# Kernel optimization log

Hardware: AMD Instinct MI355X
Metric: run time of the kernel (lower is better)

The kernel has to match this reference:

```python
import jax, jax.numpy as jnp
import numpy as np

L, D, H, HD, FF, V, R = 2, 2048, 16, 128, 5632, 32000, 16
B, S = 4, 512
LORA_SCALE = 1.4  # lora_alpha / r = (r*1.4)/r
TEMP = 0.05


def _rmsnorm(x, w):
    return x * jax.lax.rsqrt(jnp.mean(x * x, axis=-1, keepdims=True) + 1e-6) * w


def _rope(x):
    # x: [B, S, H, HD]
    half = HD // 2
    freqs = 1.0 / (10000.0 ** (jnp.arange(half, dtype=jnp.float32) / half))
    ang = jnp.arange(x.shape[1], dtype=jnp.float32)[:, None] * freqs[None, :]  # [S, half]
    cos = jnp.cos(ang)[None, :, None, :]
    sin = jnp.sin(ang)[None, :, None, :]
    x1, x2 = x[..., :half], x[..., half:]
    return jnp.concatenate([x1 * cos - x2 * sin, x1 * sin + x2 * cos], axis=-1)


def _lora(x, W, A, Bm):
    # dequantized base GEMM + low-rank LoRA path (dropout off / eval)
    return x @ W + LORA_SCALE * ((x @ A) @ Bm)


def _encode(ids, mask, emb, ln1, ln2, lnf, Wq, Aq, Bq, Wk, Ak, Bk, Wv, Av, Bv,
            Wo, Ao, Bo, Wg, Ag, Bg, Wu, Au, Bu, Wd, Ad, Bd):
    b, s = ids.shape
    h = emb[ids]  # [B,S,D]
    causal = jnp.tril(jnp.ones((s, s), dtype=bool))
    keymask = (mask > 0)[:, None, None, :]  # [B,1,1,S]
    bias = jnp.where(causal[None, None] & keymask, 0.0, -1e9).astype(h.dtype)
    for l in range(L):
        x = _rmsnorm(h, ln1[l])
        q = _lora(x, Wq[l], Aq[l], Bq[l]).reshape(b, s, H, HD)
        k = _lora(x, Wk[l], Ak[l], Bk[l]).reshape(b, s, H, HD)
        v = _lora(x, Wv[l], Av[l], Bv[l]).reshape(b, s, H, HD)
        q, k = _rope(q), _rope(k)
        scores = jnp.einsum('bqhd,bkhd->bhqk', q, k) / np.float32(np.sqrt(HD)) + bias
        attn = jax.nn.softmax(scores, axis=-1)
        o = jnp.einsum('bhqk,bkhd->bqhd', attn, v).reshape(b, s, D)
        h = h + _lora(o, Wo[l], Ao[l], Bo[l])
        x = _rmsnorm(h, ln2[l])
        g = jax.nn.silu(_lora(x, Wg[l], Ag[l], Bg[l]))
        u = _lora(x, Wu[l], Au[l], Bu[l])
        h = h + _lora(g * u, Wd[l], Ad[l], Bd[l])
    h = _rmsnorm(h, lnf)
    # last_token_pool: left-padding check, else gather at seq_len-1
    left_pad = jnp.sum(mask[:, -1]) == b
    idx = jnp.where(left_pad, s - 1, jnp.sum(mask, axis=1) - 1)
    reps = h[jnp.arange(b), idx]
    return reps / jnp.linalg.norm(reps, axis=-1, keepdims=True)  # F.normalize p=2


def setup_inputs():
    key = jax.random.key(0)
    ks = jax.random.split(key, 64)
    def nrm(k, shape, scale=0.02):
        return jax.random.normal(k, shape, dtype=jnp.float32) * scale
    inp = {}
    inp['input_ids_text'] = jax.random.randint(ks[0], (B, S), 0, V)
    lt = jax.random.randint(ks[1], (B,), S // 2, S + 1)
    inp['attention_mask_text'] = (jnp.arange(S)[None, :] < lt[:, None]).astype(jnp.int32)
    inp['input_ids_mis'] = jax.random.randint(ks[2], (B, S), 0, V)
    lm = jax.random.randint(ks[3], (B,), S // 2, S + 1)
    inp['attention_mask_mis'] = (jnp.arange(S)[None, :] < lm[:, None]).astype(jnp.int32)
    inp['emb'] = nrm(ks[4], (V, D))
    inp['ln1'] = jnp.ones((L, D), jnp.float32)
    inp['ln2'] = jnp.ones((L, D), jnp.float32)
    inp['lnf'] = jnp.ones((D,), jnp.float32)
    i = 5
    for name, (din, dout) in [('q', (D, D)), ('k', (D, D)), ('v', (D, D)), ('o', (D, D)),
                              ('g', (D, FF)), ('u', (D, FF)), ('d', (FF, D))]:
        inp['W' + name] = nrm(ks[i], (L, din, dout)); i += 1
        inp['A' + name] = nrm(ks[i], (L, din, R)); i += 1
        inp['B' + name] = nrm(ks[i], (L, R, dout), 0.002); i += 1
    return inp


def reference(input_ids_text, attention_mask_text, input_ids_mis, attention_mask_mis,
              emb, ln1, ln2, lnf, Wq, Aq, Bq, Wk, Ak, Bk, Wv, Av, Bv,
              Wo, Ao, Bo, Wg, Ag, Bg, Wu, Au, Bu, Wd, Ad, Bd):
    params = (emb, ln1, ln2, lnf, Wq, Aq, Bq, Wk, Ak, Bk, Wv, Av, Bv,
              Wo, Ao, Bo, Wg, Ag, Bg, Wu, Au, Bu, Wd, Ad, Bd)
    qr = _encode(input_ids_text, attention_mask_text, *params)
    pr = _encode(input_ids_mis, attention_mask_mis, *params)
    sims = (qr @ pr.T) / TEMP
    labels = jnp.arange(sims.shape[0])
    logp = jax.nn.log_softmax(sims, axis=-1)
    loss = -jnp.mean(jnp.take_along_axis(logp, labels[:, None], axis=1))
    return loss
```

## Files before the change

kernel.cpp:

```cpp
#include <hip/hip_runtime.h>
#include <hip/hip_bf16.h>
#include <cstddef>
#include <cstdint>

#define LNUM 2
#define DDIM 2048
#define HNUM 16
#define HDIM 128
#define FFDIM 5632
#define RNK 16
#define BB 4
#define SS 512
#define LORA_SCALE 1.4f
#define INV_TEMP 20.0f

#define BSROWS (BB * SS)
#define BSD ((size_t)BSROWS * DDIM)
#define BSFF ((size_t)BSROWS * FFDIM)
#define MAXXE ((size_t)BSROWS * FFDIM)
#define MAXWE ((size_t)FFDIM * DDIM)

typedef __attribute__((ext_vector_type(8))) short bf16x8;
typedef __attribute__((ext_vector_type(4))) float f32x4;

__device__ __forceinline__ unsigned short f2bf(float f) {
    unsigned u = __float_as_uint(f);
    unsigned r = (u + 0x7FFFu + ((u >> 16) & 1u)) >> 16;
    return (unsigned short)r;
}
__device__ __forceinline__ float bf2f(unsigned short h) {
    return __uint_as_float(((unsigned)h) << 16);
}

__global__ __launch_bounds__(256) void embed_kernel(const int* __restrict__ ids,
                                                    const float* __restrict__ emb,
                                                    float* __restrict__ H) {
    int bs = blockIdx.x;
    int id = ids[bs];
    const float4* src = (const float4*)(emb + (size_t)id * DDIM);
    float4* dst = (float4*)(H + (size_t)bs * DDIM);
    for (int i = threadIdx.x; i < DDIM / 4; i += 256) dst[i] = src[i];
}

__global__ __launch_bounds__(256) void rmsnorm_kernel(const float* __restrict__ X,
                                                      const float* __restrict__ w,
                                                      float* __restrict__ Y) {
    __shared__ float red[256];
    int row = blockIdx.x;
    const float* x = X + (size_t)row * DDIM;
    float ss = 0.f;
    for (int d = threadIdx.x; d < DDIM; d += 256) { float v = x[d]; ss += v * v; }
    red[threadIdx.x] = ss; __syncthreads();
    for (int s = 128; s > 0; s >>= 1) {
        if (threadIdx.x < s) red[threadIdx.x] += red[threadIdx.x + s];
        __syncthreads();
    }
    float scale = rsqrtf(red[0] / (float)DDIM + 1e-6f);
    float* y = Y + (size_t)row * DDIM;
    for (int d = threadIdx.x; d < DDIM; d += 256) y[d] = x[d] * scale * w[d];
}

__global__ __launch_bounds__(256) void convx_kernel(const float* __restrict__ X,
                                                    unsigned short* __restrict__ hi,
                                                    unsigned short* __restrict__ lo,
                                                    size_t n4) {
    for (size_t i = (size_t)blockIdx.x * 256 + threadIdx.x; i < n4;
         i += (size_t)gridDim.x * 256) {
        float4 v = ((const float4*)X)[i];
        ushort4 hv, lv;
        hv.x = f2bf(v.x); lv.x = f2bf(v.x - bf2f(hv.x));
        hv.y = f2bf(v.y); lv.y = f2bf(v.y - bf2f(hv.y));
        hv.z = f2bf(v.z); lv.z = f2bf(v.z - bf2f(hv.z));
        hv.w = f2bf(v.w); lv.w = f2bf(v.w - bf2f(hv.w));
        ((ushort4*)hi)[i] = hv;
        ((ushort4*)lo)[i] = lv;
    }
}

__global__ __launch_bounds__(256) void wconvt_kernel(const float* __restrict__ W,
                                                     unsigned short* __restrict__ Thi,
                                                     unsigned short* __restrict__ Tlo,
                                                     int K, int M) {
    __shared__ float tl[32][33];
    int t = threadIdx.x;
    int tr = t >> 5, tc = t & 31;
    int k0 = blockIdx.y * 32, m0 = blockIdx.x * 32;
#pragma unroll
    for (int i = 0; i < 4; ++i)
        tl[tr + i * 8][tc] = W[(size_t)(k0 + tr + i * 8) * M + m0 + tc];
    __syncthreads();
#pragma unroll
    for (int i = 0; i < 4; ++i) {
        float v = tl[tc][tr + i * 8];
        int mo = m0 + tr + i * 8, ko = k0 + tc;
        unsigned short hb = f2bf(v);
        Thi[(size_t)mo * K + ko] = hb;
        Tlo[(size_t)mo * K + ko] = f2bf(v - bf2f(hb));
    }
}

__global__ __launch_bounds__(256) void gemm_mfma_kernel(
    const unsigned short* __restrict__ Xhi, const unsigned short* __restrict__ Xlo,
    const unsigned short* __restrict__ Whi, const unsigned short* __restrict__ Wlo,
    float* __restrict__ C, int K, int M) {
    __shared__ unsigned short sAh[128 * 64];
    __shared__ unsigned short sAl[128 * 64];
    __shared__ unsigned short sBh[128 * 64];
    __shared__ unsigned short sBl[128 * 64];
    int t = threadIdx.x;
    int lane = t & 63, wave = t >> 6;
    int wm = wave >> 1, wn = wave & 1;
    int m0 = blockIdx.y * 128, n0 = blockIdx.x * 128;
    int lr = lane & 15, lk = lane >> 4;

    const unsigned short* XhA = Xhi + (size_t)m0 * K;
    const unsigned short* XlA = Xlo + (size_t)m0 * K;
    const unsigned short* WhB = Whi + (size_t)n0 * K;
    const unsigned short* WlB = Wlo + (size_t)n0 * K;

    f32x4 acc[4][4] = {};

    for (int k0 = 0; k0 < K; k0 += 64) {
#pragma unroll
        for (int i = 0; i < 4; ++i) {
            int idx = i * 256 + t;
            int rr = idx >> 3, cc = idx & 7;
            int lo = rr * 64 + ((cc ^ (rr & 7)) << 3);
            size_t ga = (size_t)rr * K + k0 + (cc << 3);
            *(int4*)(sAh + lo) = *(const int4*)(XhA + ga);
            *(int4*)(sAl + lo) = *(const int4*)(XlA + ga);
            *(int4*)(sBh + lo) = *(const int4*)(WhB + ga);
            *(int4*)(sBl + lo) = *(const int4*)(WlB + ga);
        }
        __syncthreads();
#pragma unroll
        for (int kh = 0; kh < 2; ++kh) {
            bf16x8 ah[4], al[4], bh[4], bl[4];
#pragma unroll
            for (int f = 0; f < 4; ++f) {
                int ra = wm * 64 + f * 16 + lr;
                int ca = (kh * 4 + lk) ^ (ra & 7);
                ah[f] = *(const bf16x8*)(sAh + ra * 64 + (ca << 3));
                al[f] = *(const bf16x8*)(sAl + ra * 64 + (ca << 3));
                int rb = wn * 64 + f * 16 + lr;
                int cb = (kh * 4 + lk) ^ (rb & 7);
                bh[f] = *(const bf16x8*)(sBh + rb * 64 + (cb << 3));
                bl[f] = *(const bf16x8*)(sBl + rb * 64 + (cb << 3));
            }
#pragma unroll
            for (int fm = 0; fm < 4; ++fm)
#pragma unroll
                for (int fn = 0; fn < 4; ++fn) {
                    acc[fm][fn] = __builtin_amdgcn_mfma_f32_16x16x32_bf16(
                        ah[fm], bh[fn], acc[fm][fn], 0, 0, 0);
                    acc[fm][fn] = __builtin_amdgcn_mfma_f32_16x16x32_bf16(
                        ah[fm], bl[fn], acc[fm][fn], 0, 0, 0);
                    acc[fm][fn] = __builtin_amdgcn_mfma_f32_16x16x32_bf16(
                        al[fm], bh[fn], acc[fm][fn], 0, 0, 0);
                }
        }
        __syncthreads();
    }
#pragma unroll
    for (int fm = 0; fm < 4; ++fm)
#pragma unroll
        for (int fn = 0; fn < 4; ++fn) {
            int col = n0 + wn * 64 + fn * 16 + lr;
#pragma unroll
            for (int j = 0; j < 4; ++j) {
                int row = m0 + wm * 64 + fm * 16 + lk * 4 + j;
                C[(size_t)row * M + col] = acc[fm][fn][j];
            }
        }
}

__global__ __launch_bounds__(256) void gemm16_kernel(const float* __restrict__ X,
                                                     const float* __restrict__ A,
                                                     float* __restrict__ T, int K) {
    __shared__ float part[16][17];
    int n = blockIdx.x;
    int c = threadIdx.x & 15;
    int ks = threadIdx.x >> 4;
    int kper = K / 16;
    const float* xr = X + (size_t)n * K + (size_t)ks * kper;
    const float* ac = A + (size_t)ks * kper * 16 + c;
    float acc = 0.f;
    for (int k = 0; k < kper; ++k) acc += xr[k] * ac[(size_t)k * 16];
    part[ks][c] = acc; __syncthreads();
    if (threadIdx.x < 16) {
        float s = 0.f;
#pragma unroll
        for (int i = 0; i < 16; ++i) s += part[i][threadIdx.x];
        T[(size_t)n * 16 + threadIdx.x] = s;
    }
}

__global__ __launch_bounds__(256) void lora_add_kernel(float* __restrict__ C,
                                                       const float* __restrict__ T,
                                                       const float* __restrict__ Bm,
                                                       int M) {
    __shared__ float tv[16];
    int n = blockIdx.x;
    if (threadIdx.x < 16) tv[threadIdx.x] = T[(size_t)n * 16 + threadIdx.x];
    __syncthreads();
    for (int m = threadIdx.x; m < M; m += 256) {
        float acc = 0.f;
#pragma unroll
        for (int r = 0; r < 16; ++r) acc += tv[r] * Bm[(size_t)r * M + m];
        C[(size_t)n * M + m] += LORA_SCALE * acc;
    }
}

__global__ __launch_bounds__(256) void lora_add_residual_kernel(float* __restrict__ H,
                                                                const float* __restrict__ C,
                                                                const float* __restrict__ T,
                                                                const float* __restrict__ Bm,
                                                                int M) {
    __shared__ float tv[16];
    int n = blockIdx.x;
    if (threadIdx.x < 16) tv[threadIdx.x] = T[(size_t)n * 16 + threadIdx.x];
    __syncthreads();
    for (int m = threadIdx.x; m < M; m += 256) {
        float acc = 0.f;
#pragma unroll
        for (int r = 0; r < 16; ++r) acc += tv[r] * Bm[(size_t)r * M + m];
        H[(size_t)n * M + m] += C[(size_t)n * M + m] + LORA_SCALE * acc;
    }
}

__global__ __launch_bounds__(64) void rope_kernel(float* __restrict__ X) {
    int j = threadIdx.x;
    int idx = blockIdx.x;
    int s = (idx / HNUM) % SS;
    float* p = X + (size_t)idx * HDIM;
    float freq = powf(10000.f, -(float)j / 64.f);
    float ang = (float)s * freq;
    float c = cosf(ang), sn = sinf(ang);
    float x1 = p[j], x2 = p[j + 64];
    p[j] = x1 * c - x2 * sn;
    p[j + 64] = x1 * sn + x2 * c;
}

__global__ __launch_bounds__(256) void fattn_kernel(const float* __restrict__ Q,
                                                    const float* __restrict__ Kt,
                                                    const float* __restrict__ Vt,
                                                    const int* __restrict__ mask,
                                                    float* __restrict__ O) {
    __shared__ float Qs[32 * 128];
    __shared__ float Ks[32 * 128];
    __shared__ float Vs[32 * 128];
    __shared__ float Ps[32][33];
    int t = threadIdx.x;
    int qt = blockIdx.x & 15;
    int h = (blockIdx.x >> 4) & 15;
    int b = blockIdx.x >> 8;
    int q0 = qt * 32;
    int qr = t >> 3;
    int kc4 = t & 7;

#pragma unroll
    for (int i = 0; i < 4; ++i) {
        int idx = i * 256 + t;
        int r = idx >> 5, c4 = idx & 31;
        int slot = c4 ^ (((r >> 2) & 7) << 2);
        float4 v = *(const float4*)(Q + ((((size_t)b * SS + q0 + r) * HNUM + h) * HDIM) + c4 * 4);
        *(float4*)(Qs + r * 128 + slot * 4) = v;
    }
    const float inv = 0.08838834764831845f;
    float m_run = -1e30f, l_run = 0.f;
    float4 o4[4] = {};
    int qi = q0 + qr;

    for (int kt = 0; kt <= qt; ++kt) {
        int k0 = kt * 32;
        __syncthreads();
#pragma unroll
        for (int i = 0; i < 4; ++i) {
            int idx = i * 256 + t;
            int r = idx >> 5, c4 = idx & 31;
            int slot = c4 ^ (((r >> 2) & 7) << 2);
            size_t gb = (((size_t)b * SS + k0 + r) * HNUM + h) * HDIM + c4 * 4;
            *(float4*)(Ks + r * 128 + slot * 4) = *(const float4*)(Kt + gb);
            *(float4*)(Vs + r * 128 + slot * 4) = *(const float4*)(Vt + gb);
        }
        __syncthreads();
        float s[4] = {0.f, 0.f, 0.f, 0.f};
#pragma unroll 4
        for (int d4 = 0; d4 < 32; ++d4) {
            float4 q4 = *(const float4*)(Qs + qr * 128 + (d4 ^ (((qr >> 2) & 7) << 2)) * 4);
#pragma unroll
            for (int j = 0; j < 4; ++j) {
                int kr = kc4 * 4 + j;
                float4 k4 = *(const float4*)(Ks + kr * 128 + (d4 ^ (((kr >> 2) & 7) << 2)) * 4);
                s[j] += q4.x * k4.x + q4.y * k4.y + q4.z * k4.z + q4.w * k4.w;
            }
        }
        float pmax = -1e30f;
#pragma unroll
        for (int j = 0; j < 4; ++j) {
            int kg = k0 + kc4 * 4 + j;
            bool valid = (kg <= qi) && (mask[b * SS + kg] > 0);
            s[j] = s[j] * inv + (valid ? 0.f : -1e9f);
            pmax = fmaxf(pmax, s[j]);
        }
#pragma unroll
        for (int w = 1; w < 8; w <<= 1) pmax = fmaxf(pmax, __shfl_xor(pmax, w));
        float m_new = fmaxf(m_run, pmax);
        float alpha = expf(m_run - m_new);
        float rowsum = 0.f;
#pragma unroll
        for (int j = 0; j < 4; ++j) {
            s[j] = expf(s[j] - m_new);
            rowsum += s[j];
        }
#pragma unroll
        for (int w = 1; w < 8; w <<= 1) rowsum += __shfl_xor(rowsum, w);
        l_run = l_run * alpha + rowsum;
        m_run = m_new;
#pragma unroll
        for (int j = 0; j < 4; ++j) Ps[qr][kc4 * 4 + j] = s[j];
        __syncthreads();
#pragma unroll
        for (int j4 = 0; j4 < 4; ++j4) {
            o4[j4].x *= alpha; o4[j4].y *= alpha; o4[j4].z *= alpha; o4[j4].w *= alpha;
        }
        for (int kk = 0; kk < 32; ++kk) {
            float p = Ps[qr][kk];
            int sw = ((kk >> 2) & 7) << 2;
#pragma unroll
            for (int j4 = 0; j4 < 4; ++j4) {
                float4 v4 = *(const float4*)(Vs + kk * 128 + ((kc4 * 4 + j4) ^ sw) * 4);
                o4[j4].x += p * v4.x; o4[j4].y += p * v4.y;
                o4[j4].z += p * v4.z; o4[j4].w += p * v4.w;
            }
        }
    }
    float rl = 1.f / l_run;
    size_t ob = (((size_t)b * SS + q0 + qr) * HNUM + h) * HDIM + kc4 * 16;
#pragma unroll
    for (int j4 = 0; j4 < 4; ++j4) {
        float4 r;
        r.x = o4[j4].x * rl; r.y = o4[j4].y * rl;
        r.z = o4[j4].z * rl; r.w = o4[j4].w * rl;
        *(float4*)(O + ob + j4 * 4) = r;
    }
}

__global__ __launch_bounds__(256) void silu_mul_kernel(float* __restrict__ G,
                                                       const float* __restrict__ U,
                                                       size_t n4) {
    for (size_t i = (size_t)blockIdx.x * 256 + threadIdx.x; i < n4;
         i += (size_t)gridDim.x * 256) {
        float4 g = ((const float4*)G)[i];
        float4 u = ((const float4*)U)[i];
        float4 r;
        r.x = g.x / (1.f + expf(-g.x)) * u.x;
        r.y = g.y / (1.f + expf(-g.y)) * u.y;
        r.z = g.z / (1.f + expf(-g.z)) * u.z;
        r.w = g.w / (1.f + expf(-g.w)) * u.w;
        ((float4*)G)[i] = r;
    }
}

__global__ __launch_bounds__(256) void reps_kernel(const float* __restrict__ Xn,
                                                   const int* __restrict__ mask,
                                                   float* __restrict__ reps) {
    __shared__ float red[256];
    __shared__ int sidx;
    int b = blockIdx.x;
    int ls = 0;
    for (int s = threadIdx.x; s < SS; s += 256) ls += mask[b * SS + s];
    red[threadIdx.x] = (float)ls; __syncthreads();
    for (int s2 = 128; s2 > 0; s2 >>= 1) {
        if (threadIdx.x < s2) red[threadIdx.x] += red[threadIdx.x + s2];
        __syncthreads();
    }
    if (threadIdx.x == 0) {
        int lastsum = 0;
        for (int bb = 0; bb < BB; ++bb) lastsum += mask[bb * SS + SS - 1];
        int lensum = (int)(red[0] + 0.5f);
        sidx = (lastsum == BB) ? (SS - 1) : (lensum - 1);
    }
    __syncthreads();
    const float* xr = Xn + ((size_t)b * SS + sidx) * DDIM;
    float ss = 0.f;
    for (int d = threadIdx.x; d < DDIM; d += 256) { float v = xr[d]; ss += v * v; }
    red[threadIdx.x] = ss; __syncthreads();
    for (int s2 = 128; s2 > 0; s2 >>= 1) {
        if (threadIdx.x < s2) red[threadIdx.x] += red[threadIdx.x + s2];
        __syncthreads();
    }
    float invn = rsqrtf(red[0]);
    for (int d = threadIdx.x; d < DDIM; d += 256)
        reps[(size_t)b * DDIM + d] = xr[d] * invn;
}

__global__ __launch_bounds__(256) void loss_kernel(const float* __restrict__ RQ,
                                                   const float* __restrict__ RP,
                                                   float* __restrict__ out) {
    __shared__ float red[256];
    __shared__ float sims[BB][BB];
    for (int p = 0; p < BB * BB; ++p) {
        int i = p / BB, j = p % BB;
        float acc = 0.f;
        for (int d = threadIdx.x; d < DDIM; d += 256)
            acc += RQ[(size_t)i * DDIM + d] * RP[(size_t)j * DDIM + d];
        red[threadIdx.x] = acc; __syncthreads();
        for (int s2 = 128; s2 > 0; s2 >>= 1) {
            if (threadIdx.x < s2) red[threadIdx.x] += red[threadIdx.x + s2];
            __syncthreads();
        }
        if (threadIdx.x == 0) sims[i][j] = red[0] * INV_TEMP;
        __syncthreads();
    }
    if (threadIdx.x == 0) {
        float loss = 0.f;
        for (int i = 0; i < BB; ++i) {
            float m = sims[i][0];
            for (int j = 1; j < BB; ++j) m = fmaxf(m, sims[i][j]);
            float s = 0.f;
            for (int j = 0; j < BB; ++j) s += expf(sims[i][j] - m);
            loss += -(sims[i][i] - m - logf(s));
        }
        out[0] = loss / (float)BB;
    }
}

extern "C" void kernel_launch(void* const* d_in, const int* in_sizes, int n_in,
                              void* d_out, int out_size, void* d_ws, size_t ws_size,
                              hipStream_t stream) {
    const int* ids_t = (const int*)d_in[0];
    const int* mask_t = (const int*)d_in[1];
    const int* ids_m = (const int*)d_in[2];
    const int* mask_m = (const int*)d_in[3];
    const float* emb = (const float*)d_in[4];
    const float* ln1 = (const float*)d_in[5];
    const float* ln2 = (const float*)d_in[6];
    const float* lnf = (const float*)d_in[7];
    const float* Wq = (const float*)d_in[8];
    const float* Aq = (const float*)d_in[9];
    const float* Bq = (const float*)d_in[10];
    const float* Wk = (const float*)d_in[11];
    const float* Ak = (const float*)d_in[12];
    const float* Bk = (const float*)d_in[13];
    const float* Wv = (const float*)d_in[14];
    const float* Av = (const float*)d_in[15];
    const float* Bv = (const float*)d_in[16];
    const float* Wo = (const float*)d_in[17];
    const float* Ao = (const float*)d_in[18];
    const float* Bo = (const float*)d_in[19];
    const float* Wg = (const float*)d_in[20];
    const float* Ag = (const float*)d_in[21];
    const float* Bg = (const float*)d_in[22];
    const float* Wu = (const float*)d_in[23];
    const float* Au = (const float*)d_in[24];
    const float* Bu = (const float*)d_in[25];
    const float* Wd = (const float*)d_in[26];
    const float* Ad = (const float*)d_in[27];
    const float* Bd = (const float*)d_in[28];

    float* ws = (float*)d_ws;
    float* h    = ws;
    float* x    = ws + 1 * BSD;
    float* qb   = ws + 2 * BSD;
    float* kb   = ws + 3 * BSD;
    float* vb   = ws + 4 * BSD;
    float* ob   = ws + 5 * BSD;
    float* proj = ws + 6 * BSD;
    float* gbuf = ws + 7 * BSD;
    float* ubuf = gbuf + BSFF;
    float* T    = ubuf + BSFF;
    float* repsq = T + (size_t)BSROWS * 16;
    float* repsp = repsq + BB * DDIM;
    unsigned short* xhi = (unsigned short*)(repsp + BB * DDIM);
    unsigned short* xlo = xhi + MAXXE;
    unsigned short* whi = xlo + MAXXE;
    unsigned short* wlo = whi + MAXWE;

    auto conv_x = [&](const float* Xf, size_t n) {
        hipLaunchKernelGGL(convx_kernel, dim3(1024), dim3(256), 0, stream,
                           Xf, xhi, xlo, n / 4);
    };
    auto mfma_proj = [&](const float* Wf, int K, int M, float* C) {
        hipLaunchKernelGGL(wconvt_kernel, dim3(M / 32, K / 32), dim3(256), 0, stream,
                           Wf, whi, wlo, K, M);
        hipLaunchKernelGGL(gemm_mfma_kernel, dim3(M / 128, BSROWS / 128), dim3(256),
                           0, stream, xhi, xlo, whi, wlo, C, K, M);
    };
    auto lora_tail = [&](const float* Xf, const float* Am, const float* Bm,
                         float* C, int K, int M) {
        hipLaunchKernelGGL(gemm16_kernel, dim3(BSROWS), dim3(256), 0, stream, Xf, Am, T, K);
        hipLaunchKernelGGL(lora_add_kernel, dim3(BSROWS), dim3(256), 0, stream, C, T, Bm, M);
    };
    auto lora_tail_res = [&](const float* Xf, const float* Am, const float* Bm,
                             float* Hb, float* C, int K, int M) {
        hipLaunchKernelGGL(gemm16_kernel, dim3(BSROWS), dim3(256), 0, stream, Xf, Am, T, K);
        hipLaunchKernelGGL(lora_add_residual_kernel, dim3(BSROWS), dim3(256), 0,
                           stream, Hb, C, T, Bm, M);
    };

    for (int enc = 0; enc < 2; ++enc) {
        const int* ids = enc == 0 ? ids_t : ids_m;
        const int* mask = enc == 0 ? mask_t : mask_m;
        float* reps = enc == 0 ? repsq : repsp;

        hipLaunchKernelGGL(embed_kernel, dim3(BSROWS), dim3(256), 0, stream, ids, emb, h);

        for (int l = 0; l < LNUM; ++l) {
            size_t oDD = (size_t)l * DDIM * DDIM;
            size_t oDR = (size_t)l * DDIM * RNK;
            size_t oRD = (size_t)l * RNK * DDIM;
            size_t oDF = (size_t)l * DDIM * FFDIM;
            size_t oRF = (size_t)l * RNK * FFDIM;
            size_t oFD = (size_t)l * FFDIM * DDIM;
            size_t oFR = (size_t)l * FFDIM * RNK;

            hipLaunchKernelGGL(rmsnorm_kernel, dim3(BSROWS), dim3(256), 0, stream,
                               h, ln1 + (size_t)l * DDIM, x);
            conv_x(x, BSD);
            mfma_proj(Wq + oDD, DDIM, DDIM, qb);
            lora_tail(x, Aq + oDR, Bq + oRD, qb, DDIM, DDIM);
            mfma_proj(Wk + oDD, DDIM, DDIM, kb);
            lora_tail(x, Ak + oDR, Bk + oRD, kb, DDIM, DDIM);
            mfma_proj(Wv + oDD, DDIM, DDIM, vb);
            lora_tail(x, Av + oDR, Bv + oRD, vb, DDIM, DDIM);

            hipLaunchKernelGGL(rope_kernel, dim3(BB * SS * HNUM), dim3(64), 0, stream, qb);
            hipLaunchKernelGGL(rope_kernel, dim3(BB * SS * HNUM), dim3(64), 0, stream, kb);
            hipLaunchKernelGGL(fattn_kernel, dim3(BB * HNUM * (SS / 32)), dim3(256),
                               0, stream, qb, kb, vb, mask, ob);

            conv_x(ob, BSD);
            mfma_proj(Wo + oDD, DDIM, DDIM, proj);
            lora_tail_res(ob, Ao + oDR, Bo + oRD, h, proj, DDIM, DDIM);

            hipLaunchKernelGGL(rmsnorm_kernel, dim3(BSROWS), dim3(256), 0, stream,
                               h, ln2 + (size_t)l * DDIM, x);
            conv_x(x, BSD);
            mfma_proj(Wg + oDF, DDIM, FFDIM, gbuf);
            lora_tail(x, Ag + oDR, Bg + oRF, gbuf, DDIM, FFDIM);
            mfma_proj(Wu + oDF, DDIM, FFDIM, ubuf);
            lora_tail(x, Au + oDR, Bu + oRF, ubuf, DDIM, FFDIM);

            hipLaunchKernelGGL(silu_mul_kernel, dim3(2048), dim3(256), 0, stream,
                               gbuf, ubuf, BSFF / 4);
            conv_x(gbuf, BSFF);
            mfma_proj(Wd + oFD, FFDIM, DDIM, proj);
            lora_tail_res(gbuf, Ad + oFR, Bd + oRD, h, proj, FFDIM, DDIM);
        }
        hipLaunchKernelGGL(rmsnorm_kernel, dim3(BSROWS), dim3(256), 0, stream, h, lnf, x);
        hipLaunchKernelGGL(reps_kernel, dim3(BB), dim3(256), 0, stream, x, mask, reps);
    }
    hipLaunchKernelGGL(loss_kernel, dim3(1), dim3(256), 0, stream,
                       repsq, repsp, (float*)d_out);
}
```

Before: 8.549 ms.

## Fuse bf16 split conversion into producers, use direct-to-LDS loads, retile attention

Removes the standalone hi/lo bf16 conversion kernel by folding the split into rmsnorm, the attention epilogue and silu-mul, which saves a full read and write of the activations per projection group. The MFMA GEMM now fills LDS with global_load_lds instead of staging through registers. RoPE uses a precomputed cos/sin table and handles q and k in one launch. Flash attention runs 128 threads with two query rows per thread and changes its LDS swizzles. Risks are lower attention occupancy and whether the reworked LDS layout for the direct loads still matches the swizzle the GEMM reads expect.

```diff
diff --git a/kernel.cpp b/kernel.cpp
--- a/kernel.cpp
+++ b/kernel.cpp
@@ -30,6 +30,12 @@
 }
 __device__ __forceinline__ float bf2f(unsigned short h) {
     return __uint_as_float(((unsigned)h) << 16);
+}
+
+__device__ __forceinline__ void gll16(const unsigned short* g, unsigned short* l) {
+    __builtin_amdgcn_global_load_lds(
+        (const __attribute__((address_space(1))) unsigned int*)g,
+        (__attribute__((address_space(3))) unsigned int*)l, 16, 0, 0);
 }
 
 __global__ __launch_bounds__(256) void embed_kernel(const int* __restrict__ ids,
@@ -60,20 +66,28 @@
     for (int d = threadIdx.x; d < DDIM; d += 256) y[d] = x[d] * scale * w[d];
 }
 
-__global__ __launch_bounds__(256) void convx_kernel(const float* __restrict__ X,
-                                                    unsigned short* __restrict__ hi,
-                                                    unsigned short* __restrict__ lo,
-                                                    size_t n4) {
-    for (size_t i = (size_t)blockIdx.x * 256 + threadIdx.x; i < n4;
-         i += (size_t)gridDim.x * 256) {
-        float4 v = ((const float4*)X)[i];
-        ushort4 hv, lv;
-        hv.x = f2bf(v.x); lv.x = f2bf(v.x - bf2f(hv.x));
-        hv.y = f2bf(v.y); lv.y = f2bf(v.y - bf2f(hv.y));
-        hv.z = f2bf(v.z); lv.z = f2bf(v.z - bf2f(hv.z));
-        hv.w = f2bf(v.w); lv.w = f2bf(v.w - bf2f(hv.w));
-        ((ushort4*)hi)[i] = hv;
-        ((ushort4*)lo)[i] = lv;
+__global__ __launch_bounds__(256) void rmsnorm_conv_kernel(
+    const float* __restrict__ X, const float* __restrict__ w,
+    float* __restrict__ Y, unsigned short* __restrict__ hi,
+    unsigned short* __restrict__ lo) {
+    __shared__ float red[256];
+    int row = blockIdx.x;
+    const float* x = X + (size_t)row * DDIM;
+    float ss = 0.f;
+    for (int d = threadIdx.x; d < DDIM; d += 256) { float v = x[d]; ss += v * v; }
+    red[threadIdx.x] = ss; __syncthreads();
+    for (int s = 128; s > 0; s >>= 1) {
+        if (threadIdx.x < s) red[threadIdx.x] += red[threadIdx.x + s];
+        __syncthreads();
+    }
+    float scale = rsqrtf(red[0] / (float)DDIM + 1e-6f);
+    size_t base = (size_t)row * DDIM;
+    for (int d = threadIdx.x; d < DDIM; d += 256) {
+        float y = x[d] * scale * w[d];
+        Y[base + d] = y;
+        unsigned short hb = f2bf(y);
+        hi[base + d] = hb;
+        lo[base + d] = f2bf(y - bf2f(hb));
     }
 }
 
@@ -118,19 +132,21 @@
     const unsigned short* WhB = Whi + (size_t)n0 * K;
     const unsigned short* WlB = Wlo + (size_t)n0 * K;
 
+    int srow = lane >> 3;
+    int scol = ((lane & 7) ^ srow) << 3;
+
     f32x4 acc[4][4] = {};
 
     for (int k0 = 0; k0 < K; k0 += 64) {
 #pragma unroll
         for (int i = 0; i < 4; ++i) {
-            int idx = i * 256 + t;
-            int rr = idx >> 3, cc = idx & 7;
-            int lo = rr * 64 + ((cc ^ (rr & 7)) << 3);
-            size_t ga = (size_t)rr * K + k0 + (cc << 3);
-            *(int4*)(sAh + lo) = *(const int4*)(XhA + ga);
-            *(int4*)(sAl + lo) = *(const int4*)(XlA + ga);
-            *(int4*)(sBh + lo) = *(const int4*)(WhB + ga);
-            *(int4*)(sBl + lo) = *(const int4*)(WlB + ga);
+            int rbase = wave * 32 + i * 8;
+            size_t g = (size_t)(rbase + srow) * K + k0 + scol;
+            int ldsoff = rbase * 64;
+            gll16(XhA + g, sAh + ldsoff);
+            gll16(XlA + g, sAl + ldsoff);
+            gll16(WhB + g, sBh + ldsoff);
+            gll16(WlB + g, sBl + ldsoff);
         }
         __syncthreads();
 #pragma unroll
@@ -228,24 +244,36 @@
     }
 }
 
-__global__ __launch_bounds__(64) void rope_kernel(float* __restrict__ X) {
+__global__ __launch_bounds__(64) void rope_table_kernel(float2* __restrict__ tab) {
+    int s = blockIdx.x, j = threadIdx.x;
+    float freq = powf(10000.f, -(float)j / 64.f);
+    float ang = (float)s * freq;
+    float2 cs;
+    cs.x = cosf(ang);
+    cs.y = sinf(ang);
+    tab[s * 64 + j] = cs;
+}
+
+__global__ __launch_bounds__(64) void rope_kernel(float* __restrict__ Xq,
+                                                  float* __restrict__ Xk,
+                                                  const float2* __restrict__ tab) {
     int j = threadIdx.x;
     int idx = blockIdx.x;
     int s = (idx / HNUM) % SS;
-    float* p = X + (size_t)idx * HDIM;
-    float freq = powf(10000.f, -(float)j / 64.f);
-    float ang = (float)s * freq;
-    float c = cosf(ang), sn = sinf(ang);
+    float* p = (blockIdx.y ? Xk : Xq) + (size_t)idx * HDIM;
+    float2 cs = tab[s * 64 + j];
     float x1 = p[j], x2 = p[j + 64];
-    p[j] = x1 * c - x2 * sn;
-    p[j + 64] = x1 * sn + x2 * c;
-}
-
-__global__ __launch_bounds__(256) void fattn_kernel(const float* __restrict__ Q,
+    p[j] = x1 * cs.x - x2 * cs.y;
+    p[j + 64] = x1 * cs.y + x2 * cs.x;
+}
+
+__global__ __launch_bounds__(128) void fattn_kernel(const float* __restrict__ Q,
                                                     const float* __restrict__ Kt,
                                                     const float* __restrict__ Vt,
                                                     const int* __restrict__ mask,
-                                                    float* __restrict__ O) {
+                                                    float* __restrict__ O,
+                                                    unsigned short* __restrict__ Ohi,
+                                                    unsigned short* __restrict__ Olo) {
     __shared__ float Qs[32 * 128];
     __shared__ float Ks[32 * 128];
     __shared__ float Vs[32 * 128];
@@ -255,100 +283,135 @@
     int h = (blockIdx.x >> 4) & 15;
     int b = blockIdx.x >> 8;
     int q0 = qt * 32;
-    int qr = t >> 3;
     int kc4 = t & 7;
-
-#pragma unroll
-    for (int i = 0; i < 4; ++i) {
-        int idx = i * 256 + t;
+    int qrl = t >> 3;
+    int qsw = qrl & 7;
+
+#pragma unroll
+    for (int i = 0; i < 8; ++i) {
+        int idx = i * 128 + t;
         int r = idx >> 5, c4 = idx & 31;
-        int slot = c4 ^ (((r >> 2) & 7) << 2);
-        float4 v = *(const float4*)(Q + ((((size_t)b * SS + q0 + r) * HNUM + h) * HDIM) + c4 * 4);
-        *(float4*)(Qs + r * 128 + slot * 4) = v;
+        int slot = c4 ^ (r & 7);
+        *(float4*)(Qs + r * 128 + slot * 4) =
+            *(const float4*)(Q + (((size_t)b * SS + q0 + r) * HNUM + h) * HDIM + c4 * 4);
     }
     const float inv = 0.08838834764831845f;
-    float m_run = -1e30f, l_run = 0.f;
-    float4 o4[4] = {};
-    int qi = q0 + qr;
+    float m0r = -1e30f, m1r = -1e30f, l0 = 0.f, l1 = 0.f;
+    float4 o0[4] = {}, o1[4] = {};
+    int qi0 = q0 + qrl, qi1 = q0 + qrl + 16;
 
     for (int kt = 0; kt <= qt; ++kt) {
         int k0 = kt * 32;
         __syncthreads();
 #pragma unroll
-        for (int i = 0; i < 4; ++i) {
-            int idx = i * 256 + t;
+        for (int i = 0; i < 8; ++i) {
+            int idx = i * 128 + t;
             int r = idx >> 5, c4 = idx & 31;
-            int slot = c4 ^ (((r >> 2) & 7) << 2);
             size_t gb = (((size_t)b * SS + k0 + r) * HNUM + h) * HDIM + c4 * 4;
-            *(float4*)(Ks + r * 128 + slot * 4) = *(const float4*)(Kt + gb);
-            *(float4*)(Vs + r * 128 + slot * 4) = *(const float4*)(Vt + gb);
-        }
-        __syncthreads();
-        float s[4] = {0.f, 0.f, 0.f, 0.f};
+            int kslot = c4 ^ ((r >> 2) & 7);
+            *(float4*)(Ks + r * 128 + kslot * 4) = *(const float4*)(Kt + gb);
+            *(float4*)(Vs + r * 128 + c4 * 4) = *(const float4*)(Vt + gb);
+        }
+        __syncthreads();
+        float s0[4] = {}, s1[4] = {};
 #pragma unroll 4
         for (int d4 = 0; d4 < 32; ++d4) {
-            float4 q4 = *(const float4*)(Qs + qr * 128 + (d4 ^ (((qr >> 2) & 7) << 2)) * 4);
+            float4 qa = *(const float4*)(Qs + qrl * 128 + (d4 ^ qsw) * 4);
+            float4 qb_ = *(const float4*)(Qs + (qrl + 16) * 128 + (d4 ^ qsw) * 4);
 #pragma unroll
             for (int j = 0; j < 4; ++j) {
                 int kr = kc4 * 4 + j;
-                float4 k4 = *(const float4*)(Ks + kr * 128 + (d4 ^ (((kr >> 2) & 7) << 2)) * 4);
-                s[j] += q4.x * k4.x + q4.y * k4.y + q4.z * k4.z + q4.w * k4.w;
+                float4 k4 = *(const float4*)(Ks + kr * 128 + (d4 ^ ((kr >> 2) & 7)) * 4);
+                s0[j] += qa.x * k4.x + qa.y * k4.y + qa.z * k4.z + qa.w * k4.w;
+                s1[j] += qb_.x * k4.x + qb_.y * k4.y + qb_.z * k4.z + qb_.w * k4.w;
             }
         }
-        float pmax = -1e30f;
+        float pm0 = -1e30f, pm1 = -1e30f;
 #pragma unroll
         for (int j = 0; j < 4; ++j) {
             int kg = k0 + kc4 * 4 + j;
-            bool valid = (kg <= qi) && (mask[b * SS + kg] > 0);
-            s[j] = s[j] * inv + (valid ? 0.f : -1e9f);
-            pmax = fmaxf(pmax, s[j]);
-        }
-#pragma unroll
-        for (int w = 1; w < 8; w <<= 1) pmax = fmaxf(pmax, __shfl_xor(pmax, w));
-        float m_new = fmaxf(m_run, pmax);
-        float alpha = expf(m_run - m_new);
-        float rowsum = 0.f;
+            bool km = mask[b * SS + kg] > 0;
+            s0[j] = s0[j] * inv + ((kg <= qi0 && km) ? 0.f : -1e9f);
+            s1[j] = s1[j] * inv + ((kg <= qi1 && km) ? 0.f : -1e9f);
+            pm0 = fmaxf(pm0, s0[j]);
+            pm1 = fmaxf(pm1, s1[j]);
+        }
+#pragma unroll
+        for (int w = 1; w < 8; w <<= 1) {
+            pm0 = fmaxf(pm0, __shfl_xor(pm0, w));
+            pm1 = fmaxf(pm1, __shfl_xor(pm1, w));
+        }
+        float mn0 = fmaxf(m0r, pm0), mn1 = fmaxf(m1r, pm1);
+        float a0 = expf(m0r - mn0), a1 = expf(m1r - mn1);
+        float rs0 = 0.f, rs1 = 0.f;
 #pragma unroll
         for (int j = 0; j < 4; ++j) {
-            s[j] = expf(s[j] - m_new);
-            rowsum += s[j];
-        }
-#pragma unroll
-        for (int w = 1; w < 8; w <<= 1) rowsum += __shfl_xor(rowsum, w);
-        l_run = l_run * alpha + rowsum;
-        m_run = m_new;
-#pragma unroll
-        for (int j = 0; j < 4; ++j) Ps[qr][kc4 * 4 + j] = s[j];
+            s0[j] = expf(s0[j] - mn0); rs0 += s0[j];
+            s1[j] = expf(s1[j] - mn1); rs1 += s1[j];
+        }
+#pragma unroll
+        for (int w = 1; w < 8; w <<= 1) {
+            rs0 += __shfl_xor(rs0, w);
+            rs1 += __shfl_xor(rs1, w);
+        }
+        l0 = l0 * a0 + rs0; m0r = mn0;
+        l1 = l1 * a1 + rs1; m1r = mn1;
+#pragma unroll
+        for (int j = 0; j < 4; ++j) {
+            Ps[qrl][kc4 * 4 + j] = s0[j];
+            Ps[qrl + 16][kc4 * 4 + j] = s1[j];
+        }
         __syncthreads();
 #pragma unroll
         for (int j4 = 0; j4 < 4; ++j4) {
-            o4[j4].x *= alpha; o4[j4].y *= alpha; o4[j4].z *= alpha; o4[j4].w *= alpha;
+            o0[j4].x *= a0; o0[j4].y *= a0; o0[j4].z *= a0; o0[j4].w *= a0;
+            o1[j4].x *= a1; o1[j4].y *= a1; o1[j4].z *= a1; o1[j4].w *= a1;
         }
         for (int kk = 0; kk < 32; ++kk) {
-            float p = Ps[qr][kk];
-            int sw = ((kk >> 2) & 7) << 2;
+            float p0 = Ps[qrl][kk], p1 = Ps[qrl + 16][kk];
 #pragma unroll
             for (int j4 = 0; j4 < 4; ++j4) {
-                float4 v4 = *(const float4*)(Vs + kk * 128 + ((kc4 * 4 + j4) ^ sw) * 4);
-                o4[j4].x += p * v4.x; o4[j4].y += p * v4.y;
-                o4[j4].z += p * v4.z; o4[j4].w += p * v4.w;
+                float4 v4 = *(const float4*)(Vs + kk * 128 + j4 * 32 + kc4 * 4);
+                o0[j4].x += p0 * v4.x; o0[j4].y += p0 * v4.y;
+                o0[j4].z += p0 * v4.z; o0[j4].w += p0 * v4.w;
+                o1[j4].x += p1 * v4.x; o1[j4].y += p1 * v4.y;
+                o1[j4].z += p1 * v4.z; o1[j4].w += p1 * v4.w;
             }
         }
     }
-    float rl = 1.f / l_run;
-    size_t ob = (((size_t)b * SS + q0 + qr) * HNUM + h) * HDIM + kc4 * 16;
+    float rl0 = 1.f / l0, rl1 = 1.f / l1;
+    size_t ob0 = (((size_t)b * SS + qi0) * HNUM + h) * HDIM;
+    size_t ob1 = (((size_t)b * SS + qi1) * HNUM + h) * HDIM;
 #pragma unroll
     for (int j4 = 0; j4 < 4; ++j4) {
-        float4 r;
-        r.x = o4[j4].x * rl; r.y = o4[j4].y * rl;
-        r.z = o4[j4].z * rl; r.w = o4[j4].w * rl;
-        *(float4*)(O + ob + j4 * 4) = r;
-    }
-}
-
-__global__ __launch_bounds__(256) void silu_mul_kernel(float* __restrict__ G,
-                                                       const float* __restrict__ U,
-                                                       size_t n4) {
+        float4 r0, r1;
+        r0.x = o0[j4].x * rl0; r0.y = o0[j4].y * rl0;
+        r0.z = o0[j4].z * rl0; r0.w = o0[j4].w * rl0;
+        r1.x = o1[j4].x * rl1; r1.y = o1[j4].y * rl1;
+        r1.z = o1[j4].z * rl1; r1.w = o1[j4].w * rl1;
+        size_t i0 = ob0 + j4 * 32 + kc4 * 4;
+        size_t i1 = ob1 + j4 * 32 + kc4 * 4;
+        *(float4*)(O + i0) = r0;
+        *(float4*)(O + i1) = r1;
+        ushort4 h0, l0v, h1, l1v;
+        h0.x = f2bf(r0.x); l0v.x = f2bf(r0.x - bf2f(h0.x));
+        h0.y = f2bf(r0.y); l0v.y = f2bf(r0.y - bf2f(h0.y));
+        h0.z = f2bf(r0.z); l0v.z = f2bf(r0.z - bf2f(h0.z));
+        h0.w = f2bf(r0.w); l0v.w = f2bf(r0.w - bf2f(h0.w));
+        h1.x = f2bf(r1.x); l1v.x = f2bf(r1.x - bf2f(h1.x));
+        h1.y = f2bf(r1.y); l1v.y = f2bf(r1.y - bf2f(h1.y));
+        h1.z = f2bf(r1.z); l1v.z = f2bf(r1.z - bf2f(h1.z));
+        h1.w = f2bf(r1.w); l1v.w = f2bf(r1.w - bf2f(h1.w));
+        *(ushort4*)(Ohi + i0) = h0;
+        *(ushort4*)(Olo + i0) = l0v;
+        *(ushort4*)(Ohi + i1) = h1;
+        *(ushort4*)(Olo + i1) = l1v;
+    }
+}
+
+__global__ __launch_bounds__(256) void silu_mul_conv_kernel(
+    float* __restrict__ G, const float* __restrict__ U,
+    unsigned short* __restrict__ hi, unsigned short* __restrict__ lo, size_t n4) {
     for (size_t i = (size_t)blockIdx.x * 256 + threadIdx.x; i < n4;
          i += (size_t)gridDim.x * 256) {
         float4 g = ((const float4*)G)[i];
@@ -359,6 +422,13 @@
         r.z = g.z / (1.f + expf(-g.z)) * u.z;
         r.w = g.w / (1.f + expf(-g.w)) * u.w;
         ((float4*)G)[i] = r;
+        ushort4 hv, lv;
+        hv.x = f2bf(r.x); lv.x = f2bf(r.x - bf2f(hv.x));
+        hv.y = f2bf(r.y); lv.y = f2bf(r.y - bf2f(hv.y));
+        hv.z = f2bf(r.z); lv.z = f2bf(r.z - bf2f(hv.z));
+        hv.w = f2bf(r.w); lv.w = f2bf(r.w - bf2f(hv.w));
+        ((ushort4*)hi)[i] = hv;
+        ((ushort4*)lo)[i] = lv;
     }
 }
 
@@ -472,15 +542,14 @@
     float* T    = ubuf + BSFF;
     float* repsq = T + (size_t)BSROWS * 16;
     float* repsp = repsq + BB * DDIM;
-    unsigned short* xhi = (unsigned short*)(repsp + BB * DDIM);
+    float2* rtab = (float2*)(repsp + BB * DDIM);
+    unsigned short* xhi = (unsigned short*)(rtab + SS * 64);
     unsigned short* xlo = xhi + MAXXE;
     unsigned short* whi = xlo + MAXXE;
     unsigned short* wlo = whi + MAXWE;
 
-    auto conv_x = [&](const float* Xf, size_t n) {
-        hipLaunchKernelGGL(convx_kernel, dim3(1024), dim3(256), 0, stream,
-                           Xf, xhi, xlo, n / 4);
-    };
+    hipLaunchKernelGGL(rope_table_kernel, dim3(SS), dim3(64), 0, stream, rtab);
+
     auto mfma_proj = [&](const float* Wf, int K, int M, float* C) {
         hipLaunchKernelGGL(wconvt_kernel, dim3(M / 32, K / 32), dim3(256), 0, stream,
                            Wf, whi, wlo, K, M);
@@ -515,9 +584,8 @@
             size_t oFD = (size_t)l * FFDIM * DDIM;
             size_t oFR = (size_t)l * FFDIM * RNK;
 
-            hipLaunchKernelGGL(rmsnorm_kernel, dim3(BSROWS), dim3(256), 0, stream,
-                               h, ln1 + (size_t)l * DDIM, x);
-            conv_x(x, BSD);
+            hipLaunchKernelGGL(rmsnorm_conv_kernel, dim3(BSROWS), dim3(256), 0, stream,
+                               h, ln1 + (size_t)l * DDIM, x, xhi, xlo);
             mfma_proj(Wq + oDD, DDIM, DDIM, qb);
             lora_tail(x, Aq + oDR, Bq + oRD, qb, DDIM, DDIM);
             mfma_proj(Wk + oDD, DDIM, DDIM, kb);
@@ -525,26 +593,23 @@
             mfma_proj(Wv + oDD, DDIM, DDIM, vb);
             lora_tail(x, Av + oDR, Bv + oRD, vb, DDIM, DDIM);
 
-            hipLaunchKernelGGL(rope_kernel, dim3(BB * SS * HNUM), dim3(64), 0, stream, qb);
-            hipLaunchKernelGGL(rope_kernel, dim3(BB * SS * HNUM), dim3(64), 0, stream, kb);
-            hipLaunchKernelGGL(fattn_kernel, dim3(BB * HNUM * (SS / 32)), dim3(256),
-                               0, stream, qb, kb, vb, mask, ob);
-
-            conv_x(ob, BSD);
+            hipLaunchKernelGGL(rope_kernel, dim3(BB * SS * HNUM, 2), dim3(64), 0,
+                               stream, qb, kb, rtab);
+            hipLaunchKernelGGL(fattn_kernel, dim3(BB * HNUM * (SS / 32)), dim3(128),
+                               0, stream, qb, kb, vb, mask, ob, xhi, xlo);
+
             mfma_proj(Wo + oDD, DDIM, DDIM, proj);
             lora_tail_res(ob, Ao + oDR, Bo + oRD, h, proj, DDIM, DDIM);
 
-            hipLaunchKernelGGL(rmsnorm_kernel, dim3(BSROWS), dim3(256), 0, stream,
-                               h, ln2 + (size_t)l * DDIM, x);
-            conv_x(x, BSD);
+            hipLaunchKernelGGL(rmsnorm_conv_kernel, dim3(BSROWS), dim3(256), 0, stream,
+                               h, ln2 + (size_t)l * DDIM, x, xhi, xlo);
             mfma_proj(Wg + oDF, DDIM, FFDIM, gbuf);
             lora_tail(x, Ag + oDR, Bg + oRF, gbuf, DDIM, FFDIM);
             mfma_proj(Wu + oDF, DDIM, FFDIM, ubuf);
             lora_tail(x, Au + oDR, Bu + oRF, ubuf, DDIM, FFDIM);
 
-            hipLaunchKernelGGL(silu_mul_kernel, dim3(2048), dim3(256), 0, stream,
-                               gbuf, ubuf, BSFF / 4);
-            conv_x(gbuf, BSFF);
+            hipLaunchKernelGGL(silu_mul_conv_kernel, dim3(2048), dim3(256), 0, stream,
+                               gbuf, ubuf, xhi, xlo, BSFF / 4);
             mfma_proj(Wd + oFD, FFDIM, DDIM, proj);
             lora_tail_res(gbuf, Ad + oFR, Bd + oRD, h, proj, FFDIM, DDIM);
         }
```

Measured after the change: 8.086 ms. -5.4%, faster.
